# Performance work log

Hardware: AMD Instinct MI355X
Metric: run time of the kernel (lower is better)

The kernel has to match this reference:

```python
import jax, jax.numpy as jnp
import numpy as np

B, S, E, A = 8, 127, 512, 256  # batch, seq (pre-sentinel), encoder dim, arc representation dim

_BRANCHES = ["sib_head", "sib_dep", "cop_head", "cop_dep", "gp_head", "gp_dep", "gp_head_dep"]


def setup_inputs() -> dict:
    key = jax.random.key(0)
    ks = jax.random.split(key, 16)
    d = {
        "x": jax.random.normal(ks[0], (B, S, E), jnp.float32),
        "pos_tags": jax.random.randint(ks[1], (B, S), 0, 48),
        "mask": jnp.ones((B, S), jnp.int32),
    }
    for i, n in enumerate(_BRANCHES):
        d[f"W_{n}"] = jax.random.normal(ks[2 + i], (E, A), jnp.float32) * (1.0 / np.sqrt(E))
        d[f"b_{n}"] = jnp.zeros((A,), jnp.float32)
    for i, n in enumerate(["sib", "cop", "gp"]):
        d[f"U_{n}"] = jax.random.normal(ks[9 + i], (A, A, A), jnp.float32) * (1.0 / A)
    d["sentinel"] = jax.random.normal(ks[12], (E,), jnp.float32)
    return d


def _tri(u, v, w, U):
    # trilinear (triaffine) score: s[b,i,j,k] = sum_{a,c,d} u[b,i,a] U[a,c,d] v[b,j,c] w[b,k,d]
    t = jnp.einsum('bia,acd->bicd', u, U)       # [B, n, A, A]
    t = jnp.einsum('bicd,bjc->bijd', t, v)      # [B, n, n, A]
    return jnp.einsum('bijd,bkd->bijk', t, w)   # [B, n, n, n]


def reference(x, pos_tags, mask,
              W_sib_head, b_sib_head, W_sib_dep, b_sib_dep,
              W_cop_head, b_cop_head, W_cop_dep, b_cop_dep,
              W_gp_head, b_gp_head, W_gp_dep, b_gp_dep,
              W_gp_head_dep, b_gp_head_dep,
              U_sib, U_cop, U_gp, sentinel):
    b, _, e = x.shape
    # prepend head sentinel token
    h = jnp.concatenate([jnp.broadcast_to(sentinel, (b, 1, e)), x], axis=1)  # [B, n, E]
    mask_full = jnp.concatenate([jnp.ones((b, 1), mask.dtype), mask], axis=1)
    elu = jax.nn.elu
    sib_head = elu(h @ W_sib_head + b_sib_head)
    sib_dep = elu(h @ W_sib_dep + b_sib_dep)
    cop_head = elu(h @ W_cop_head + b_cop_head)
    cop_dep = elu(h @ W_cop_dep + b_cop_dep)
    gp_head = elu(h @ W_gp_head + b_gp_head)
    gp_dep = elu(h @ W_gp_dep + b_gp_dep)
    gp_head_dep = elu(h @ W_gp_head_dep + b_gp_head_dep)
    sib = _tri(sib_head, sib_dep, sib_dep, U_sib)
    cop = _tri(cop_head, cop_dep, cop_head, U_cop)
    gp = _tri(gp_head, gp_head_dep, gp_dep, U_gp)
    return sib, cop, gp, mask_full
```

## Files before the change

kernel.cpp:

```cpp
#include <hip/hip_runtime.h>
#include <math.h>

#define N_TOK 128
#define ADIM  256
#define EDIM  512
#define BSZ   8
#define NSQ   65536
#define DCH   128
#define NCH   (DCH * 256)
#define PAD   40

typedef short bf16x8 __attribute__((ext_vector_type(8)));
typedef float f32x4  __attribute__((ext_vector_type(4)));
#define MFMA_BF16(a, b, c) __builtin_amdgcn_mfma_f32_16x16x32_bf16((a), (b), (c), 0, 0, 0)

__device__ inline short f2bf(float f) {
  union { float f; unsigned u; } v; v.f = f;
  unsigned r = v.u + 0x7fff + ((v.u >> 16) & 1);
  return (short)(r >> 16);
}

struct ProjArgs {
  const float* W[7];
  const float* b[7];
};

__global__ __launch_bounds__(256) void proj_kernel(
    const float* __restrict__ x, const float* __restrict__ sentinel,
    ProjArgs args, short* __restrict__ proj)
{
  const int p  = blockIdx.y;
  const int m0 = blockIdx.x * 8;
  const int tid = threadIdx.x;
  __shared__ float hs[8][EDIM];
  #pragma unroll
  for (int q = 0; q < 16; ++q) {
    int idx = tid + q * 256;
    int r = idx >> 9, c = idx & 511;
    int m = m0 + r, b = m >> 7, i = m & 127;
    hs[r][c] = (i == 0) ? sentinel[c] : x[((size_t)(b * 127) + (i - 1)) * EDIM + c];
  }
  __syncthreads();
  const float* W = args.W[p];
  float bias = args.b[p][tid];
  float acc[8];
  #pragma unroll
  for (int r = 0; r < 8; ++r) acc[r] = bias;
  #pragma unroll 4
  for (int k = 0; k < EDIM; ++k) {
    float wv = W[(size_t)k * ADIM + tid];
    #pragma unroll
    for (int r = 0; r < 8; ++r) acc[r] = fmaf(hs[r][k], wv, acc[r]);
  }
  short* outp = proj + ((size_t)p * (BSZ * N_TOK) + m0) * ADIM + tid;
  #pragma unroll
  for (int r = 0; r < 8; ++r) {
    float v = acc[r];
    v = v > 0.f ? v : expm1f(v);
    outp[(size_t)r * ADIM] = f2bf(v);
  }
}

__global__ __launch_bounds__(256) void permU(
    const float* __restrict__ U, short* __restrict__ Ut, int d0c)
{
  __shared__ float tile[64][69];
  const int c  = blockIdx.x;
  const int a0 = blockIdx.y * 64;
  const int d0 = blockIdx.z * 64;
  const int t  = threadIdx.x;
  {
    int ar = t >> 4, ds4 = (t & 15) * 4;
    #pragma unroll
    for (int q = 0; q < 4; ++q) {
      int a = ar + q * 16;
      float4 v = *(const float4*)&U[(size_t)(a0 + a) * NSQ + c * 256 + d0c + d0 + ds4];
      tile[a][ds4] = v.x; tile[a][ds4 + 1] = v.y;
      tile[a][ds4 + 2] = v.z; tile[a][ds4 + 3] = v.w;
    }
  }
  __syncthreads();
  {
    int dr = t >> 4, as4 = (t & 15) * 4;
    #pragma unroll
    for (int q = 0; q < 4; ++q) {
      int d = dr + q * 16;
      ushort4 o;
      o.x = (unsigned short)f2bf(tile[as4 + 0][d]);
      o.y = (unsigned short)f2bf(tile[as4 + 1][d]);
      o.z = (unsigned short)f2bf(tile[as4 + 2][d]);
      o.w = (unsigned short)f2bf(tile[as4 + 3][d]);
      *(ushort4*)&Ut[((size_t)(d0 + d) * 256 + c) * 256 + a0 + as4] = o;
    }
  }
}

__global__ __launch_bounds__(256) void gemm_t1(
    const short* __restrict__ A,
    const short* __restrict__ Ut,
    short* __restrict__ C)
{
  __shared__ short As[128][PAD];
  __shared__ short Bs[128][PAD];
  const int tid = threadIdx.x;
  const int wave = tid >> 6, lane = tid & 63;
  const int ln15 = lane & 15, quad = lane >> 4;
  const int m0 = blockIdx.x * 128, n0 = blockIdx.y * 128;
  const int wm = (wave & 1) * 64, wn = (wave >> 1) * 64;
  f32x4 acc[4][4] = {};
  for (int kt = 0; kt < ADIM; kt += 32) {
    __syncthreads();
    #pragma unroll
    for (int p = 0; p < 2; ++p) {
      int q = tid + p * 256;
      int r = q >> 2, s = q & 3;
      *(uint4*)&As[r][s * 8] = *(const uint4*)&A [(size_t)(m0 + r) * ADIM + kt + s * 8];
      *(uint4*)&Bs[r][s * 8] = *(const uint4*)&Ut[(size_t)(n0 + r) * ADIM + kt + s * 8];
    }
    __syncthreads();
    bf16x8 af[4], bfr[4];
    #pragma unroll
    for (int r = 0; r < 4; ++r)  af[r]  = *(bf16x8*)&As[wm + r * 16 + ln15][quad * 8];
    #pragma unroll
    for (int c2 = 0; c2 < 4; ++c2) bfr[c2] = *(bf16x8*)&Bs[wn + c2 * 16 + ln15][quad * 8];
    #pragma unroll
    for (int r = 0; r < 4; ++r)
      #pragma unroll
      for (int c2 = 0; c2 < 4; ++c2)
        acc[r][c2] = MFMA_BF16(bfr[c2], af[r], acc[r][c2]);
  }
  #pragma unroll
  for (int r = 0; r < 4; ++r)
    #pragma unroll
    for (int c2 = 0; c2 < 4; ++c2) {
      int m = m0 + wm + r * 16 + ln15;
      int n = n0 + wn + c2 * 16 + quad * 4;
      ushort4 o;
      o.x = (unsigned short)f2bf(acc[r][c2][0]);
      o.y = (unsigned short)f2bf(acc[r][c2][1]);
      o.z = (unsigned short)f2bf(acc[r][c2][2]);
      o.w = (unsigned short)f2bf(acc[r][c2][3]);
      *(ushort4*)&C[(size_t)m * NCH + n] = o;
    }
}

__global__ __launch_bounds__(256) void gemm_t2(
    const short* __restrict__ t1c,
    const short* __restrict__ projv,
    short* __restrict__ t2,
    int d0c)
{
  __shared__ short As[128][PAD];
  __shared__ short Bs[128][PAD];
  const int tid = threadIdx.x;
  const int wave = tid >> 6, lane = tid & 63;
  const int ln15 = lane & 15, quad = lane >> 4;
  const int n0 = blockIdx.x * 128;
  const int bl = blockIdx.y;
  const short* Bt = t1c + (size_t)bl * N_TOK * NCH;
  const short* Av = projv + (size_t)bl * N_TOK * ADIM;
  const int wm = (wave & 1) * 64, wn = (wave >> 1) * 64;
  f32x4 acc[4][4] = {};
  for (int kt = 0; kt < ADIM; kt += 32) {
    __syncthreads();
    #pragma unroll
    for (int p = 0; p < 2; ++p) {
      int q = tid + p * 256;
      int r = q >> 2, s = q & 3;
      *(uint4*)&As[r][s * 8] = *(const uint4*)&Av[(size_t)r * ADIM + kt + s * 8];
      *(uint4*)&Bs[r][s * 8] = *(const uint4*)&Bt[(size_t)(n0 + r) * ADIM + kt + s * 8];
    }
    __syncthreads();
    bf16x8 af[4], bfr[4];
    #pragma unroll
    for (int r = 0; r < 4; ++r)  af[r]  = *(bf16x8*)&As[wm + r * 16 + ln15][quad * 8];
    #pragma unroll
    for (int c2 = 0; c2 < 4; ++c2) bfr[c2] = *(bf16x8*)&Bs[wn + c2 * 16 + ln15][quad * 8];
    #pragma unroll
    for (int r = 0; r < 4; ++r)
      #pragma unroll
      for (int c2 = 0; c2 < 4; ++c2)
        acc[r][c2] = MFMA_BF16(bfr[c2], af[r], acc[r][c2]);
  }
  const int i = n0 >> 7;
  short* ob = t2 + (size_t)bl * (N_TOK * N_TOK * ADIM) + (size_t)i * (N_TOK * ADIM) + d0c;
  #pragma unroll
  for (int r = 0; r < 4; ++r)
    #pragma unroll
    for (int c2 = 0; c2 < 4; ++c2) {
      int j  = wm + r * 16 + ln15;
      int dl = wn + c2 * 16 + quad * 4;
      ushort4 o;
      o.x = (unsigned short)f2bf(acc[r][c2][0]);
      o.y = (unsigned short)f2bf(acc[r][c2][1]);
      o.z = (unsigned short)f2bf(acc[r][c2][2]);
      o.w = (unsigned short)f2bf(acc[r][c2][3]);
      *(ushort4*)&ob[(size_t)j * ADIM + dl] = o;
    }
}

__global__ __launch_bounds__(256) void gemm_s(
    const short* __restrict__ t2,
    const short* __restrict__ projw,
    float* __restrict__ out)
{
  __shared__ short As[128][PAD];
  __shared__ short Bs[128][PAD];
  const int tid = threadIdx.x;
  const int wave = tid >> 6, lane = tid & 63;
  const int ln15 = lane & 15, quad = lane >> 4;
  const int m0 = blockIdx.x * 128;
  const int bl = blockIdx.y;
  const short* At = t2 + (size_t)bl * (N_TOK * N_TOK * ADIM);
  const short* Bw = projw + (size_t)bl * N_TOK * ADIM;
  float* ob = out + (size_t)bl * N_TOK * N_TOK * N_TOK + (size_t)m0 * N_TOK;
  const int wm = (wave & 1) * 64, wn = (wave >> 1) * 64;
  f32x4 acc[4][4] = {};
  for (int kt = 0; kt < ADIM; kt += 32) {
    __syncthreads();
    #pragma unroll
    for (int p = 0; p < 2; ++p) {
      int q = tid + p * 256;
      int r = q >> 2, s = q & 3;
      *(uint4*)&As[r][s * 8] = *(const uint4*)&At[(size_t)(m0 + r) * ADIM + kt + s * 8];
      *(uint4*)&Bs[r][s * 8] = *(const uint4*)&Bw[(size_t)r * ADIM + kt + s * 8];
    }
    __syncthreads();
    bf16x8 af[4], bfr[4];
    #pragma unroll
    for (int r = 0; r < 4; ++r)  af[r]  = *(bf16x8*)&As[wm + r * 16 + ln15][quad * 8];
    #pragma unroll
    for (int c2 = 0; c2 < 4; ++c2) bfr[c2] = *(bf16x8*)&Bs[wn + c2 * 16 + ln15][quad * 8];
    #pragma unroll
    for (int r = 0; r < 4; ++r)
      #pragma unroll
      for (int c2 = 0; c2 < 4; ++c2)
        acc[r][c2] = MFMA_BF16(bfr[c2], af[r], acc[r][c2]);
  }
  #pragma unroll
  for (int r = 0; r < 4; ++r)
    #pragma unroll
    for (int c2 = 0; c2 < 4; ++c2) {
      int m = wm + r * 16 + ln15;
      int k = wn + c2 * 16 + quad * 4;
      *(f32x4*)&ob[(size_t)m * N_TOK + k] = acc[r][c2];
    }
}

__global__ void mask_kernel(const int* __restrict__ mask, float* __restrict__ out) {
  int idx = blockIdx.x * 256 + threadIdx.x;
  if (idx < BSZ * N_TOK) {
    int b = idx >> 7, i = idx & 127;
    out[idx] = (i == 0) ? 1.0f : (float)mask[b * 127 + i - 1];
  }
}

extern "C" void kernel_launch(void* const* d_in, const int* in_sizes, int n_in,
                              void* d_out, int out_size, void* d_ws, size_t ws_size,
                              hipStream_t stream)
{
  const float* x    = (const float*)d_in[0];
  const int*   mask = (const int*)d_in[2];
  ProjArgs pa;
  for (int p = 0; p < 7; ++p) {
    pa.W[p] = (const float*)d_in[3 + 2 * p];
    pa.b[p] = (const float*)d_in[4 + 2 * p];
  }
  const float* Us[3] = {(const float*)d_in[17], (const float*)d_in[18],
                        (const float*)d_in[19]};
  const float* sentinel = (const float*)d_in[20];

  short* proj = (short*)d_ws;
  const size_t ut_off = 4u << 20;
  const size_t t1_off = ut_off + ((size_t)NCH * 256 * 2);
  const size_t t2_off = t1_off + ((size_t)1024 * NCH * 2);
  short* Utc = (short*)((char*)d_ws + ut_off);
  short* t1c = (short*)((char*)d_ws + t1_off);
  short* t2  = (short*)((char*)d_ws + t2_off);

  proj_kernel<<<dim3(128, 7), 256, 0, stream>>>(x, sentinel, pa, proj);

  const int u_idx[3] = {0, 2, 4};
  const int v_idx[3] = {1, 3, 6};
  const int w_idx[3] = {1, 2, 5};
  float* outp = (float*)d_out;

  for (int sc = 0; sc < 3; ++sc) {
    for (int ch = 0; ch < 256 / DCH; ++ch) {
      const int d0c = ch * DCH;
      permU<<<dim3(256, 4, DCH / 64), 256, 0, stream>>>(Us[sc], Utc, d0c);
      gemm_t1<<<dim3(8, NCH / 128), 256, 0, stream>>>(
          proj + (size_t)u_idx[sc] * 1024 * ADIM, Utc, t1c);
      gemm_t2<<<dim3(128, 8), 256, 0, stream>>>(
          t1c, proj + (size_t)v_idx[sc] * 1024 * ADIM, t2, d0c);
    }
    gemm_s<<<dim3(128, 8), 256, 0, stream>>>(
        t2, proj + (size_t)w_idx[sc] * 1024 * ADIM,
        outp + (size_t)sc * BSZ * N_TOK * N_TOK * N_TOK);
  }
  mask_kernel<<<dim3(4), 256, 0, stream>>>(
      mask, outp + (size_t)3 * BSZ * N_TOK * N_TOK * N_TOK);
}
```

Before: 969.4 us.

## Use direct global-to-LDS loads with XOR swizzle and drop d-chunking of t1

All three MFMA GEMM kernels now stage tiles with global_load_lds (direct global-to-LDS DMA) into unpadded LDS tiles. The tiles use an XOR swizzle on the 16-byte column slot to avoid bank conflicts. Separately, the D dimension is no longer split into two 128-wide chunks, so each score type needs one permU, one t1 GEMM and one t2 GEMM launch instead of two each. This halves launch count and raises per-launch parallelism, at the cost of a workspace t1 buffer twice as large (1024x65536 bf16).

```diff
diff --git a/kernel.cpp b/kernel.cpp
--- a/kernel.cpp
+++ b/kernel.cpp
@@ -6,9 +6,6 @@
 #define EDIM  512
 #define BSZ   8
 #define NSQ   65536
-#define DCH   128
-#define NCH   (DCH * 256)
-#define PAD   40
 
 typedef short bf16x8 __attribute__((ext_vector_type(8)));
 typedef float f32x4  __attribute__((ext_vector_type(4)));
@@ -18,6 +15,12 @@
   union { float f; unsigned u; } v; v.f = f;
   unsigned r = v.u + 0x7fff + ((v.u >> 16) & 1);
   return (short)(r >> 16);
+}
+
+typedef const __attribute__((address_space(1))) unsigned int* gas_ptr;
+typedef __attribute__((address_space(3))) unsigned int* las_ptr;
+__device__ __forceinline__ void gload16(const void* g, void* l) {
+  __builtin_amdgcn_global_load_lds((gas_ptr)g, (las_ptr)l, 16, 0, 0);
 }
 
 struct ProjArgs {
@@ -62,7 +65,7 @@
 }
 
 __global__ __launch_bounds__(256) void permU(
-    const float* __restrict__ U, short* __restrict__ Ut, int d0c)
+    const float* __restrict__ U, short* __restrict__ Ut)
 {
   __shared__ float tile[64][69];
   const int c  = blockIdx.x;
@@ -74,7 +77,7 @@
     #pragma unroll
     for (int q = 0; q < 4; ++q) {
       int a = ar + q * 16;
-      float4 v = *(const float4*)&U[(size_t)(a0 + a) * NSQ + c * 256 + d0c + d0 + ds4];
+      float4 v = *(const float4*)&U[(size_t)(a0 + a) * NSQ + c * 256 + d0 + ds4];
       tile[a][ds4] = v.x; tile[a][ds4 + 1] = v.y;
       tile[a][ds4 + 2] = v.z; tile[a][ds4 + 3] = v.w;
     }
@@ -95,34 +98,35 @@
   }
 }
 
+
 __global__ __launch_bounds__(256) void gemm_t1(
     const short* __restrict__ A,
     const short* __restrict__ Ut,
     short* __restrict__ C)
 {
-  __shared__ short As[128][PAD];
-  __shared__ short Bs[128][PAD];
+  __shared__ short As[128 * 32];
+  __shared__ short Bs[128 * 32];
   const int tid = threadIdx.x;
   const int wave = tid >> 6, lane = tid & 63;
   const int ln15 = lane & 15, quad = lane >> 4;
   const int m0 = blockIdx.x * 128, n0 = blockIdx.y * 128;
   const int wm = (wave & 1) * 64, wn = (wave >> 1) * 64;
+  const int q0 = tid,        r0 = q0 >> 2, s0 = (q0 & 3) ^ ((r0 >> 1) & 3);
+  const int q1 = tid + 256,  r1 = q1 >> 2, s1 = (q1 & 3) ^ ((r1 >> 1) & 3);
+  const int rdoff = ((quad ^ ((ln15 >> 1) & 3)) << 3);
   f32x4 acc[4][4] = {};
   for (int kt = 0; kt < ADIM; kt += 32) {
     __syncthreads();
-    #pragma unroll
-    for (int p = 0; p < 2; ++p) {
-      int q = tid + p * 256;
-      int r = q >> 2, s = q & 3;
-      *(uint4*)&As[r][s * 8] = *(const uint4*)&A [(size_t)(m0 + r) * ADIM + kt + s * 8];
-      *(uint4*)&Bs[r][s * 8] = *(const uint4*)&Ut[(size_t)(n0 + r) * ADIM + kt + s * 8];
-    }
+    gload16(&A [(size_t)(m0 + r0) * ADIM + kt + s0 * 8], &As[q0 * 8]);
+    gload16(&A [(size_t)(m0 + r1) * ADIM + kt + s1 * 8], &As[q1 * 8]);
+    gload16(&Ut[(size_t)(n0 + r0) * ADIM + kt + s0 * 8], &Bs[q0 * 8]);
+    gload16(&Ut[(size_t)(n0 + r1) * ADIM + kt + s1 * 8], &Bs[q1 * 8]);
     __syncthreads();
     bf16x8 af[4], bfr[4];
     #pragma unroll
-    for (int r = 0; r < 4; ++r)  af[r]  = *(bf16x8*)&As[wm + r * 16 + ln15][quad * 8];
-    #pragma unroll
-    for (int c2 = 0; c2 < 4; ++c2) bfr[c2] = *(bf16x8*)&Bs[wn + c2 * 16 + ln15][quad * 8];
+    for (int r = 0; r < 4; ++r)  af[r]  = *(bf16x8*)&As[(wm + r * 16 + ln15) * 32 + rdoff];
+    #pragma unroll
+    for (int c2 = 0; c2 < 4; ++c2) bfr[c2] = *(bf16x8*)&Bs[(wn + c2 * 16 + ln15) * 32 + rdoff];
     #pragma unroll
     for (int r = 0; r < 4; ++r)
       #pragma unroll
@@ -140,62 +144,62 @@
       o.y = (unsigned short)f2bf(acc[r][c2][1]);
       o.z = (unsigned short)f2bf(acc[r][c2][2]);
       o.w = (unsigned short)f2bf(acc[r][c2][3]);
-      *(ushort4*)&C[(size_t)m * NCH + n] = o;
+      *(ushort4*)&C[(size_t)m * NSQ + n] = o;
     }
 }
 
 __global__ __launch_bounds__(256) void gemm_t2(
-    const short* __restrict__ t1c,
+    const short* __restrict__ t1,
     const short* __restrict__ projv,
-    short* __restrict__ t2,
-    int d0c)
-{
-  __shared__ short As[128][PAD];
-  __shared__ short Bs[128][PAD];
+    short* __restrict__ t2)
+{
+  __shared__ short As[128 * 32];
+  __shared__ short Bs[128 * 32];
   const int tid = threadIdx.x;
   const int wave = tid >> 6, lane = tid & 63;
   const int ln15 = lane & 15, quad = lane >> 4;
   const int n0 = blockIdx.x * 128;
   const int bl = blockIdx.y;
-  const short* Bt = t1c + (size_t)bl * N_TOK * NCH;
+  const short* Bt = t1 + (size_t)bl * N_TOK * NSQ;
   const short* Av = projv + (size_t)bl * N_TOK * ADIM;
   const int wm = (wave & 1) * 64, wn = (wave >> 1) * 64;
+  const int q0 = tid,        r0 = q0 >> 2, s0 = (q0 & 3) ^ ((r0 >> 1) & 3);
+  const int q1 = tid + 256,  r1 = q1 >> 2, s1 = (q1 & 3) ^ ((r1 >> 1) & 3);
+  const int rdoff = ((quad ^ ((ln15 >> 1) & 3)) << 3);
   f32x4 acc[4][4] = {};
   for (int kt = 0; kt < ADIM; kt += 32) {
     __syncthreads();
-    #pragma unroll
-    for (int p = 0; p < 2; ++p) {
-      int q = tid + p * 256;
-      int r = q >> 2, s = q & 3;
-      *(uint4*)&As[r][s * 8] = *(const uint4*)&Av[(size_t)r * ADIM + kt + s * 8];
-      *(uint4*)&Bs[r][s * 8] = *(const uint4*)&Bt[(size_t)(n0 + r) * ADIM + kt + s * 8];
-    }
+    gload16(&Av[(size_t)r0 * ADIM + kt + s0 * 8],        &As[q0 * 8]);
+    gload16(&Av[(size_t)r1 * ADIM + kt + s1 * 8],        &As[q1 * 8]);
+    gload16(&Bt[(size_t)(n0 + r0) * ADIM + kt + s0 * 8], &Bs[q0 * 8]);
+    gload16(&Bt[(size_t)(n0 + r1) * ADIM + kt + s1 * 8], &Bs[q1 * 8]);
     __syncthreads();
     bf16x8 af[4], bfr[4];
     #pragma unroll
-    for (int r = 0; r < 4; ++r)  af[r]  = *(bf16x8*)&As[wm + r * 16 + ln15][quad * 8];
-    #pragma unroll
-    for (int c2 = 0; c2 < 4; ++c2) bfr[c2] = *(bf16x8*)&Bs[wn + c2 * 16 + ln15][quad * 8];
+    for (int r = 0; r < 4; ++r)  af[r]  = *(bf16x8*)&As[(wm + r * 16 + ln15) * 32 + rdoff];
+    #pragma unroll
+    for (int c2 = 0; c2 < 4; ++c2) bfr[c2] = *(bf16x8*)&Bs[(wn + c2 * 16 + ln15) * 32 + rdoff];
     #pragma unroll
     for (int r = 0; r < 4; ++r)
       #pragma unroll
       for (int c2 = 0; c2 < 4; ++c2)
         acc[r][c2] = MFMA_BF16(bfr[c2], af[r], acc[r][c2]);
   }
-  const int i = n0 >> 7;
-  short* ob = t2 + (size_t)bl * (N_TOK * N_TOK * ADIM) + (size_t)i * (N_TOK * ADIM) + d0c;
+  const int i     = n0 >> 8;
+  const int dbase = n0 & 255;
+  short* ob = t2 + (size_t)bl * (N_TOK * N_TOK * ADIM) + (size_t)i * (N_TOK * ADIM);
   #pragma unroll
   for (int r = 0; r < 4; ++r)
     #pragma unroll
     for (int c2 = 0; c2 < 4; ++c2) {
-      int j  = wm + r * 16 + ln15;
-      int dl = wn + c2 * 16 + quad * 4;
+      int j = wm + r * 16 + ln15;
+      int d = dbase + wn + c2 * 16 + quad * 4;
       ushort4 o;
       o.x = (unsigned short)f2bf(acc[r][c2][0]);
       o.y = (unsigned short)f2bf(acc[r][c2][1]);
       o.z = (unsigned short)f2bf(acc[r][c2][2]);
       o.w = (unsigned short)f2bf(acc[r][c2][3]);
-      *(ushort4*)&ob[(size_t)j * ADIM + dl] = o;
+      *(ushort4*)&ob[(size_t)j * ADIM + d] = o;
     }
 }
 
@@ -204,8 +208,8 @@
     const short* __restrict__ projw,
     float* __restrict__ out)
 {
-  __shared__ short As[128][PAD];
-  __shared__ short Bs[128][PAD];
+  __shared__ short As[128 * 32];
+  __shared__ short Bs[128 * 32];
   const int tid = threadIdx.x;
   const int wave = tid >> 6, lane = tid & 63;
   const int ln15 = lane & 15, quad = lane >> 4;
@@ -215,22 +219,22 @@
   const short* Bw = projw + (size_t)bl * N_TOK * ADIM;
   float* ob = out + (size_t)bl * N_TOK * N_TOK * N_TOK + (size_t)m0 * N_TOK;
   const int wm = (wave & 1) * 64, wn = (wave >> 1) * 64;
+  const int q0 = tid,        r0 = q0 >> 2, s0 = (q0 & 3) ^ ((r0 >> 1) & 3);
+  const int q1 = tid + 256,  r1 = q1 >> 2, s1 = (q1 & 3) ^ ((r1 >> 1) & 3);
+  const int rdoff = ((quad ^ ((ln15 >> 1) & 3)) << 3);
   f32x4 acc[4][4] = {};
   for (int kt = 0; kt < ADIM; kt += 32) {
     __syncthreads();
-    #pragma unroll
-    for (int p = 0; p < 2; ++p) {
-      int q = tid + p * 256;
-      int r = q >> 2, s = q & 3;
-      *(uint4*)&As[r][s * 8] = *(const uint4*)&At[(size_t)(m0 + r) * ADIM + kt + s * 8];
-      *(uint4*)&Bs[r][s * 8] = *(const uint4*)&Bw[(size_t)r * ADIM + kt + s * 8];
-    }
+    gload16(&At[(size_t)(m0 + r0) * ADIM + kt + s0 * 8], &As[q0 * 8]);
+    gload16(&At[(size_t)(m0 + r1) * ADIM + kt + s1 * 8], &As[q1 * 8]);
+    gload16(&Bw[(size_t)r0 * ADIM + kt + s0 * 8],        &Bs[q0 * 8]);
+    gload16(&Bw[(size_t)r1 * ADIM + kt + s1 * 8],        &Bs[q1 * 8]);
     __syncthreads();
     bf16x8 af[4], bfr[4];
     #pragma unroll
-    for (int r = 0; r < 4; ++r)  af[r]  = *(bf16x8*)&As[wm + r * 16 + ln15][quad * 8];
-    #pragma unroll
-    for (int c2 = 0; c2 < 4; ++c2) bfr[c2] = *(bf16x8*)&Bs[wn + c2 * 16 + ln15][quad * 8];
+    for (int r = 0; r < 4; ++r)  af[r]  = *(bf16x8*)&As[(wm + r * 16 + ln15) * 32 + rdoff];
+    #pragma unroll
+    for (int c2 = 0; c2 < 4; ++c2) bfr[c2] = *(bf16x8*)&Bs[(wn + c2 * 16 + ln15) * 32 + rdoff];
     #pragma unroll
     for (int r = 0; r < 4; ++r)
       #pragma unroll
@@ -272,11 +276,11 @@
 
   short* proj = (short*)d_ws;
   const size_t ut_off = 4u << 20;
-  const size_t t1_off = ut_off + ((size_t)NCH * 256 * 2);
-  const size_t t2_off = t1_off + ((size_t)1024 * NCH * 2);
-  short* Utc = (short*)((char*)d_ws + ut_off);
-  short* t1c = (short*)((char*)d_ws + t1_off);
-  short* t2  = (short*)((char*)d_ws + t2_off);
+  const size_t t1_off = ut_off + ((size_t)NSQ * ADIM * 2);
+  const size_t t2_off = t1_off + ((size_t)1024 * NSQ * 2);
+  short* Ut = (short*)((char*)d_ws + ut_off);
+  short* t1 = (short*)((char*)d_ws + t1_off);
+  short* t2 = (short*)((char*)d_ws + t2_off);
 
   proj_kernel<<<dim3(128, 7), 256, 0, stream>>>(x, sentinel, pa, proj);
 
@@ -286,14 +290,11 @@
   float* outp = (float*)d_out;
 
   for (int sc = 0; sc < 3; ++sc) {
-    for (int ch = 0; ch < 256 / DCH; ++ch) {
-      const int d0c = ch * DCH;
-      permU<<<dim3(256, 4, DCH / 64), 256, 0, stream>>>(Us[sc], Utc, d0c);
-      gemm_t1<<<dim3(8, NCH / 128), 256, 0, stream>>>(
-          proj + (size_t)u_idx[sc] * 1024 * ADIM, Utc, t1c);
-      gemm_t2<<<dim3(128, 8), 256, 0, stream>>>(
-          t1c, proj + (size_t)v_idx[sc] * 1024 * ADIM, t2, d0c);
-    }
+    permU<<<dim3(256, 4, 4), 256, 0, stream>>>(Us[sc], Ut);
+    gemm_t1<<<dim3(8, 512), 256, 0, stream>>>(
+        proj + (size_t)u_idx[sc] * 1024 * ADIM, Ut, t1);
+    gemm_t2<<<dim3(256, 8), 256, 0, stream>>>(
+        t1, proj + (size_t)v_idx[sc] * 1024 * ADIM, t2);
     gemm_s<<<dim3(128, 8), 256, 0, stream>>>(
         t2, proj + (size_t)w_idx[sc] * 1024 * ADIM,
         outp + (size_t)sc * BSZ * N_TOK * N_TOK * N_TOK);
```

New measurement: 885.7 us. 1.09x faster.
